# Kernel tuning notes

Hardware: AMD Instinct MI355X
Metric: run time of the kernel (lower is better)

Reference implementation:

```python
import jax, jax.numpy as jnp
import numpy as np

HEADS = 12
NUM_IMS = 1
SCALE = 1.0


def _layernorm(x, g, b, eps=1e-5):
    m = jnp.mean(x, axis=-1, keepdims=True)
    v = jnp.var(x, axis=-1, keepdims=True)
    return (x - m) / jnp.sqrt(v + eps) * g + b


def _mha(q, k, v):
    # q: [B, Nq, C], k/v: [B, Nk, C]; multi-head softmax attention
    B, Nq, C = q.shape
    d = C // HEADS
    qh = q.reshape(B, Nq, HEADS, d)
    kh = k.reshape(B, k.shape[1], HEADS, d)
    vh = v.reshape(B, v.shape[1], HEADS, d)
    sim = jnp.einsum('bihd,bjhd->bhij', qh, kh) * (d ** -0.5)
    w = jax.nn.softmax(sim, axis=-1)
    out = jnp.einsum('bhij,bjhd->bihd', w, vh)
    return out.reshape(B, Nq, C)


def _forward(hidden_states, encoder_hidden_states, ln1_g, ln1_b, ln2_g, ln2_b,
             sa_wq, sa_wk, sa_wv, sa_wo, sa_wo_b, ff_ln_g, ff_ln_b, ff_w1, ff_w2,
             alpha_attn, alpha_dense, ca_wq, ca_wk, ca_wv, ca_wo, ca_wo_b):
    B, N, C = hidden_states.shape
    end_pos = encoder_hidden_states.shape[1] - 16 * NUM_IMS
    text = encoder_hidden_states[:, :end_pos]   # [B, Lt, C]
    face = encoder_hidden_states[:, end_pos:]   # [B, 16, C]

    x = hidden_states
    # gated self-attention over visual tokens + face tokens
    x_ln = _layernorm(x, ln1_g, ln1_b)
    face_ln = _layernorm(face, ln1_g, ln1_b)
    comb = jnp.concatenate([x_ln, face_ln], axis=1)  # [B, N+16, C]
    attn_out = _mha(comb @ sa_wq, comb @ sa_wk, comb @ sa_wv) @ sa_wo + sa_wo_b
    attn_out = attn_out[:, :N]
    x = x + SCALE * jnp.tanh(alpha_attn) * attn_out

    # gated GEGLU feed-forward (norm2 outside, FF has its own LayerNorm)
    h = _layernorm(x, ln2_g, ln2_b)
    h = _layernorm(h, ff_ln_g, ff_ln_b)
    h = h @ ff_w1                                 # [B, N, 2*inner]
    a, gate = jnp.split(h, 2, axis=-1)
    h = (a * jax.nn.gelu(gate, approximate=False)) @ ff_w2
    x = x + SCALE * jnp.tanh(alpha_dense) * h

    residual = x
    # cross attention against text tokens (diffusers Attention, residual_connection=True)
    out = _mha(x @ ca_wq, text @ ca_wk, text @ ca_wv) @ ca_wo + ca_wo_b
    return out + residual


def setup_inputs() -> dict:
    key = jax.random.key(0)
    ks = jax.random.split(key, 16)
    B, N, C, L, INNER = 2, 1024, 768, 77 + 16 * NUM_IMS, 3072
    W = 0.02
    return {
        'hidden_states': jax.random.normal(ks[0], (B, N, C), jnp.float32),
        'encoder_hidden_states': jax.random.normal(ks[1], (B, L, C), jnp.float32),
        'ln1_g': jnp.ones((C,), jnp.float32),
        'ln1_b': jnp.zeros((C,), jnp.float32),
        'ln2_g': jnp.ones((C,), jnp.float32),
        'ln2_b': jnp.zeros((C,), jnp.float32),
        'sa_wq': jax.random.normal(ks[2], (C, C), jnp.float32) * W,
        'sa_wk': jax.random.normal(ks[3], (C, C), jnp.float32) * W,
        'sa_wv': jax.random.normal(ks[4], (C, C), jnp.float32) * W,
        'sa_wo': jax.random.normal(ks[5], (C, C), jnp.float32) * W,
        'sa_wo_b': jnp.zeros((C,), jnp.float32),
        'ff_ln_g': jnp.ones((C,), jnp.float32),
        'ff_ln_b': jnp.zeros((C,), jnp.float32),
        'ff_w1': jax.random.normal(ks[6], (C, 2 * INNER), jnp.float32) * W,
        'ff_w2': jax.random.normal(ks[7], (INNER, C), jnp.float32) * W,
        'alpha_attn': jnp.float32(0.5),
        'alpha_dense': jnp.float32(0.5),
        'ca_wq': jax.random.normal(ks[8], (C, C), jnp.float32) * W,
        'ca_wk': jax.random.normal(ks[9], (C, C), jnp.float32) * W,
        'ca_wv': jax.random.normal(ks[10], (C, C), jnp.float32) * W,
        'ca_wo': jax.random.normal(ks[11], (C, C), jnp.float32) * W,
        'ca_wo_b': jnp.zeros((C,), jnp.float32),
    }


def reference(hidden_states, encoder_hidden_states, ln1_g, ln1_b, ln2_g, ln2_b,
              sa_wq, sa_wk, sa_wv, sa_wo, sa_wo_b, ff_ln_g, ff_ln_b, ff_w1, ff_w2,
              alpha_attn, alpha_dense, ca_wq, ca_wk, ca_wv, ca_wo, ca_wo_b):
    return _forward(hidden_states, encoder_hidden_states, ln1_g, ln1_b, ln2_g, ln2_b,
                    sa_wq, sa_wk, sa_wv, sa_wo, sa_wo_b, ff_ln_g, ff_ln_b, ff_w1, ff_w2,
                    alpha_attn, alpha_dense, ca_wq, ca_wk, ca_wv, ca_wo, ca_wo_b)
```

## Files before the change

### kernel.cpp

```cpp
#include <hip/hip_runtime.h>
#include <hip/hip_bf16.h>
#include <math.h>


#define C_DIM 768
#define B_DIM 2
#define N_DIM 1024
#define NC_DIM 1040
#define L_DIM 93
#define TEXT_LEN 77
#define INNER 3072
#define MNX 1572864

typedef unsigned short ushort_t;
typedef __bf16 bf16x8 __attribute__((ext_vector_type(8)));
typedef float f32x4 __attribute__((ext_vector_type(4)));

__device__ __forceinline__ ushort_t f2b(float f) {
  __hip_bfloat16 h = __float2bfloat16(f);
  return *(ushort_t*)&h;
}
__device__ __forceinline__ float b2f(ushort_t u) {
  __hip_bfloat16 h = *(__hip_bfloat16*)&u;
  return __bfloat162float(h);
}

__device__ __forceinline__ void g2lds16(const void* g, void* l) {
  __builtin_amdgcn_global_load_lds(
      (const __attribute__((address_space(1))) unsigned int*)g,
      (__attribute__((address_space(3))) unsigned int*)l, 16, 0, 0);
}

#define WX1    0u
#define WX2    6291456u
#define WQKV   12582912u
#define WBB1   22167552u
#define WG     47333376u
#define WS1    59916288u
#define WTEXT  63062016u
#define WATT2  63298560u
#define WWQKV  66444288u
#define WWO    69983232u
#define WW1    71162880u
#define WW2    80600064u
#define WCAWQ  85318656u
#define WCAKV  86498304u
#define WCAWO  88857600u
#define WVT1   90037248u
#define WVT2   93379584u
#define WOPART WBB1
#define WLBUF  WG
#define WATTN  (WG + 524288u)
#define WPART  WBB1

__device__ __forceinline__ float block_sum(float v, float* sh) {
#pragma unroll
  for (int o = 32; o > 0; o >>= 1) v += __shfl_down(v, o);
  int lane = threadIdx.x & 63, w = threadIdx.x >> 6;
  if (lane == 0) sh[w] = v;
  __syncthreads();
  float r = sh[0] + sh[1] + sh[2] + sh[3];
  __syncthreads();
  return r;
}

struct WtDesc {
  const float* src[10];
  ushort_t*    dst[10];
  int K[10];
  int N[10];
  int tilesX[10];
  int ileave[10];
  int start[11];
};

__global__ __launch_bounds__(256)
void prep_kernel(WtDesc d,
                 const float* __restrict__ x, const float* __restrict__ enc,
                 const float* __restrict__ g, const float* __restrict__ b,
                 ushort_t* __restrict__ comb, ushort_t* __restrict__ text) {
  __shared__ float tile[64][65];
  int bid = blockIdx.x;
  int nwt = d.start[10];
  if (bid >= nwt) {
    int r = bid - nwt;
    if (r >= B_DIM * NC_DIM) {
      int i = r - B_DIM * NC_DIM;
      int bb = i / TEXT_LEN, j = i % TEXT_LEN;
      const float* src = enc + ((size_t)bb * L_DIM + j) * C_DIM;
      ushort_t* dst = text + (size_t)i * C_DIM;
#pragma unroll
      for (int l = 0; l < 3; ++l) {
        int c = threadIdx.x + l * 256;
        dst[c] = f2b(src[c]);
      }
      return;
    }
    float* sh = &tile[0][0];
    int bb = r / NC_DIM, i = r % NC_DIM;
    const float* src = (i < N_DIM)
        ? (x   + ((size_t)bb * N_DIM + i) * C_DIM)
        : (enc + ((size_t)bb * L_DIM + TEXT_LEN + (i - N_DIM)) * C_DIM);
    float v[3];
#pragma unroll
    for (int j = 0; j < 3; ++j) v[j] = src[threadIdx.x + j * 256];
    float mean = block_sum(v[0] + v[1] + v[2], sh) * (1.f / C_DIM);
    float sq = 0.f;
#pragma unroll
    for (int j = 0; j < 3; ++j) { float dd = v[j] - mean; sq += dd * dd; }
    float rstd = rsqrtf(block_sum(sq, sh) * (1.f / C_DIM) + 1e-5f);
    ushort_t* dst = comb + (size_t)r * C_DIM;
#pragma unroll
    for (int j = 0; j < 3; ++j) {
      int c = threadIdx.x + j * 256;
      dst[c] = f2b((v[j] - mean) * rstd * g[c] + b[c]);
    }
    return;
  }
  int j = 0;
  while (j < 9 && bid >= d.start[j + 1]) ++j;
  int ti = bid - d.start[j];
  int K = d.K[j], N = d.N[j];
  int n0 = (ti % d.tilesX[j]) * 64, k0 = (ti / d.tilesX[j]) * 64;
  const float* in = d.src[j];
  ushort_t* out = d.dst[j];
  int il = d.ileave[j];
  int t = threadIdx.x;
#pragma unroll
  for (int p = 0; p < 16; ++p) {
    int idx = t + p * 256;
    int r = idx >> 6, c = idx & 63;
    tile[r][c] = in[(size_t)(k0 + r) * N + n0 + c];
  }
  __syncthreads();
#pragma unroll
  for (int p = 0; p < 16; ++p) {
    int idx = t + p * 256;
    int r = idx >> 6, c = idx & 63;
    int nrow = n0 + r;
    int dstrow = il ? ((nrow < INNER) ? (nrow * 2) : ((nrow - INNER) * 2 + 1)) : nrow;
    out[(size_t)dstrow * K + k0 + c] = f2b(tile[c][r]);
  }
}

__global__ __launch_bounds__(256)
void gemm_bf16(const ushort_t* __restrict__ A, const ushort_t* __restrict__ Bt,
               ushort_t* __restrict__ Ob, ushort_t* __restrict__ Og,
               int M, int N, int K) {
  __shared__ ushort_t sA[2][128 * 32];
  __shared__ ushort_t sB[2][128 * 32];
  int t = threadIdx.x;
  int w = t >> 6, ln = t & 63;
  int m0 = blockIdx.y * 128, n0 = blockIdx.x * 128;
  int wm = (w >> 1) * 64, wn = (w & 1) * 64;
  int lr = ln & 15, lq = ln >> 4;
  int seg_r = ln >> 2, seg_c = (ln & 3) * 8;

  f32x4 acc[4][4];
#pragma unroll
  for (int mi = 0; mi < 4; ++mi)
#pragma unroll
    for (int ni = 0; ni < 4; ++ni) acc[mi][ni] = (f32x4){0.f, 0.f, 0.f, 0.f};

#define STAGE(k0_, buf_)                                                     \
  do {                                                                       \
    _Pragma("unroll") for (int l = 0; l < 2; ++l) {                          \
      int s = w * 2 + l;                                                     \
      int arow = m0 + s * 16 + seg_r;                                        \
      arow = arow < M ? arow : M - 1;                                        \
      g2lds16(A + (size_t)arow * K + (k0_) + seg_c, &sA[buf_][s * 512]);     \
      int nrow = n0 + s * 16 + seg_r;                                        \
      g2lds16(Bt + (size_t)nrow * K + (k0_) + seg_c, &sB[buf_][s * 512]);    \
    }                                                                        \
  } while (0)

  STAGE(0, 0);
  __syncthreads();
  int cur = 0;
  for (int k0 = 0; k0 < K; k0 += 32) {
    if (k0 + 32 < K) STAGE(k0 + 32, cur ^ 1);
    bf16x8 af[4], bfr[4];
#pragma unroll
    for (int mi = 0; mi < 4; ++mi)
      af[mi] = *(const bf16x8*)&sA[cur][(wm + mi * 16 + lr) * 32 + lq * 8];
#pragma unroll
    for (int ni = 0; ni < 4; ++ni)
      bfr[ni] = *(const bf16x8*)&sB[cur][(wn + ni * 16 + lr) * 32 + lq * 8];
#pragma unroll
    for (int mi = 0; mi < 4; ++mi)
#pragma unroll
      for (int ni = 0; ni < 4; ++ni)
        acc[mi][ni] = __builtin_amdgcn_mfma_f32_16x16x32_bf16(
            af[mi], bfr[ni], acc[mi][ni], 0, 0, 0);
    __syncthreads();
    cur ^= 1;
  }
#undef STAGE

  if (Og) {
#pragma unroll
    for (int mi = 0; mi < 4; ++mi)
#pragma unroll
      for (int ni = 0; ni < 4; ++ni) {
        int col = n0 + wn + ni * 16 + lr;
#pragma unroll
        for (int r = 0; r < 4; ++r) {
          float val = acc[mi][ni][r];
          float other = __shfl_xor(val, 1);
          if (!(lr & 1)) {
            float a = val, gate = other;
            float ge = 0.5f * gate * (1.f + erff(gate * 0.70710678118654752f));
            int row = m0 + wm + mi * 16 + lq * 4 + r;
            Og[(size_t)row * INNER + (col >> 1)] = f2b(a * ge);
          }
        }
      }
  } else {
#pragma unroll
    for (int mi = 0; mi < 4; ++mi)
#pragma unroll
      for (int ni = 0; ni < 4; ++ni) {
        int col = n0 + wn + ni * 16 + lr;
#pragma unroll
        for (int r = 0; r < 4; ++r) {
          int row = m0 + wm + mi * 16 + lq * 4 + r;
          if (row < M) Ob[(size_t)row * N + col] = f2b(acc[mi][ni][r]);
        }
      }
  }
}

__global__ __launch_bounds__(256)
void gemm64(const ushort_t* __restrict__ A, const ushort_t* __restrict__ Bt,
            float* __restrict__ Out, ushort_t* __restrict__ Ob,
            float* __restrict__ Part,
            int M, int N, int K, int Ksplit,
            const float* __restrict__ bias, const float* __restrict__ res,
            const float* __restrict__ alphaPtr,
            const ushort_t* __restrict__ A2, const ushort_t* __restrict__ Bt2,
            ushort_t* __restrict__ Ob2, int M2, int N2, int ybreak) {
  __shared__ ushort_t sA[2][4096];
  __shared__ ushort_t sB[2][4096];
  int by = blockIdx.y;
  if (A2 && by >= ybreak) {
    if ((int)blockIdx.x * 64 >= N2) return;
    A = A2; Bt = Bt2; Ob = Ob2; M = M2; N = N2;
    Out = nullptr; Part = nullptr; bias = nullptr; res = nullptr; alphaPtr = nullptr;
    by -= ybreak;
  }
  int t = threadIdx.x;
  int w = t >> 6, ln = t & 63;
  int m0 = by * 64, n0 = blockIdx.x * 64;
  int wm = (w >> 1) * 32, wn = (w & 1) * 32;
  int lr = ln & 15, lq = ln >> 4;
  int srow = (w & 1) * 32 + (ln >> 2);
  int skoff = (w >> 1) * 32 + (ln & 3) * 8;
  int kbeg = blockIdx.z * Ksplit;
  int kend = kbeg + Ksplit; if (kend > K) kend = K;

  f32x4 acc[2][2];
#pragma unroll
  for (int mi = 0; mi < 2; ++mi)
#pragma unroll
    for (int ni = 0; ni < 2; ++ni) acc[mi][ni] = (f32x4){0.f, 0.f, 0.f, 0.f};

#define STG64(k0_, buf_)                                                      \
  do {                                                                        \
    _Pragma("unroll") for (int i = 0; i < 2; ++i) {                           \
      int ar = m0 + srow + i * 16; ar = ar < M ? ar : M - 1;                  \
      g2lds16(A + (size_t)ar * K + (k0_) + skoff,                             \
              (char*)sA + (buf_) * 8192 + w * 2048 + i * 1024);               \
      int nr = n0 + srow + i * 16;                                            \
      g2lds16(Bt + (size_t)nr * K + (k0_) + skoff,                            \
              (char*)sB + (buf_) * 8192 + w * 2048 + i * 1024);               \
    }                                                                         \
  } while (0)

  STG64(kbeg, 0);
  __syncthreads();
  int cur = 0;
  for (int k0 = kbeg; k0 < kend; k0 += 64) {
    if (k0 + 64 < kend) STG64(k0 + 64, cur ^ 1);
#pragma unroll
    for (int s = 0; s < 2; ++s) {
      bf16x8 a0 = *(const bf16x8*)&sA[cur][s * 2048 + (wm + lr) * 32 + lq * 8];
      bf16x8 a1 = *(const bf16x8*)&sA[cur][s * 2048 + (wm + 16 + lr) * 32 + lq * 8];
      bf16x8 b0 = *(const bf16x8*)&sB[cur][s * 2048 + (wn + lr) * 32 + lq * 8];
      bf16x8 b1 = *(const bf16x8*)&sB[cur][s * 2048 + (wn + 16 + lr) * 32 + lq * 8];
      acc[0][0] = __builtin_amdgcn_mfma_f32_16x16x32_bf16(a0, b0, acc[0][0], 0, 0, 0);
      acc[0][1] = __builtin_amdgcn_mfma_f32_16x16x32_bf16(a0, b1, acc[0][1], 0, 0, 0);
      acc[1][0] = __builtin_amdgcn_mfma_f32_16x16x32_bf16(a1, b0, acc[1][0], 0, 0, 0);
      acc[1][1] = __builtin_amdgcn_mfma_f32_16x16x32_bf16(a1, b1, acc[1][1], 0, 0, 0);
    }
    __syncthreads();
    cur ^= 1;
  }
#undef STG64

  if (Part) {
    float* P = Part + (size_t)blockIdx.z * M * N;
#pragma unroll
    for (int mi = 0; mi < 2; ++mi)
#pragma unroll
      for (int ni = 0; ni < 2; ++ni) {
        int col = n0 + wn + ni * 16 + lr;
#pragma unroll
        for (int r = 0; r < 4; ++r) {
          int row = m0 + wm + mi * 16 + lq * 4 + r;
          if (row < M) P[(size_t)row * N + col] = acc[mi][ni][r];
        }
      }
  } else {
    float f = alphaPtr ? tanhf(alphaPtr[0]) : 1.0f;
#pragma unroll
    for (int mi = 0; mi < 2; ++mi)
#pragma unroll
      for (int ni = 0; ni < 2; ++ni) {
        int col = n0 + wn + ni * 16 + lr;
        float bv = bias ? bias[col] : 0.f;
#pragma unroll
        for (int r = 0; r < 4; ++r) {
          int row = m0 + wm + mi * 16 + lq * 4 + r;
          if (row < M) {
            float val = acc[mi][ni][r] + bv;
            if (res) val = res[(size_t)row * N + col] + f * val;
            if (Out) Out[(size_t)row * N + col] = val;
            if (Ob)  Ob[(size_t)row * N + col] = f2b(val);
          }
        }
      }
  }
}

__global__ __launch_bounds__(256)
void splitk_epi(const float* __restrict__ Part, int nz, float* __restrict__ Out,
                ushort_t* __restrict__ Ob, int MN, int N,
                const float* __restrict__ bias, const float* __restrict__ res,
                const float* __restrict__ alphaPtr) {
  int idx = (blockIdx.x * 256 + threadIdx.x) * 4;
  if (idx >= MN) return;
  float f = alphaPtr ? tanhf(alphaPtr[0]) : 1.0f;
  float v[4] = {0.f, 0.f, 0.f, 0.f};
  for (int z = 0; z < nz; ++z) {
    float4 a = *(const float4*)&Part[(size_t)z * MN + idx];
    v[0] += a.x; v[1] += a.y; v[2] += a.z; v[3] += a.w;
  }
  if (bias) {
    int col = idx % N;
    float4 bb = *(const float4*)&bias[col];
    v[0] += bb.x; v[1] += bb.y; v[2] += bb.z; v[3] += bb.w;
  }
  if (res) {
    float4 rr = *(const float4*)&res[idx];
    v[0] = rr.x + f * v[0]; v[1] = rr.y + f * v[1];
    v[2] = rr.z + f * v[2]; v[3] = rr.w + f * v[3];
  }
  if (Out) *(float4*)&Out[idx] = make_float4(v[0], v[1], v[2], v[3]);
  if (Ob) {
    ushort4 o;
    o.x = f2b(v[0]); o.y = f2b(v[1]); o.z = f2b(v[2]); o.w = f2b(v[3]);
    *(ushort4*)&Ob[idx] = o;
  }
}

__global__ __launch_bounds__(256)
void woepi_ln_kernel(const float* __restrict__ Part, int nz,
                     const float* __restrict__ bias, const float* __restrict__ xres,
                     const float* __restrict__ alphaPtr, float* __restrict__ x1,
                     const float* __restrict__ g1, const float* __restrict__ b1,
                     const float* __restrict__ g2, const float* __restrict__ b2,
                     ushort_t* __restrict__ hh) {
  __shared__ float sh[4];
  int row = blockIdx.x;
  float f = tanhf(alphaPtr[0]);
  float v[3];
#pragma unroll
  for (int j = 0; j < 3; ++j) {
    int c = threadIdx.x + j * 256;
    float s = 0.f;
    for (int z = 0; z < nz; ++z) s += Part[(size_t)z * MNX + (size_t)row * C_DIM + c];
    s += bias[c];
    float xv = xres[(size_t)row * C_DIM + c] + f * s;
    x1[(size_t)row * C_DIM + c] = xv;
    v[j] = xv;
  }
  float mean = block_sum(v[0] + v[1] + v[2], sh) * (1.f / C_DIM);
  float sq = 0.f;
#pragma unroll
  for (int j = 0; j < 3; ++j) { float d = v[j] - mean; sq += d * d; }
  float rstd = rsqrtf(block_sum(sq, sh) * (1.f / C_DIM) + 1e-5f);
  float y[3];
#pragma unroll
  for (int j = 0; j < 3; ++j) {
    int c = threadIdx.x + j * 256;
    y[j] = (v[j] - mean) * rstd * g1[c] + b1[c];
  }
  float mean2 = block_sum(y[0] + y[1] + y[2], sh) * (1.f / C_DIM);
  sq = 0.f;
#pragma unroll
  for (int j = 0; j < 3; ++j) { float d = y[j] - mean2; sq += d * d; }
  float rstd2 = rsqrtf(block_sum(sq, sh) * (1.f / C_DIM) + 1e-5f);
#pragma unroll
  for (int j = 0; j < 3; ++j) {
    int c = threadIdx.x + j * 256;
    hh[(size_t)row * C_DIM + c] = f2b((y[j] - mean2) * rstd2 * g2[c] + b2[c]);
  }
}

__global__ __launch_bounds__(256)
void vtrans_kernel(const ushort_t* __restrict__ V, ushort_t* __restrict__ Vt,
                   int rows_per_b, int stride, int Nk, int Nkp,
                   const ushort_t* __restrict__ V2, ushort_t* __restrict__ Vt2,
                   int rows2, int stride2, int Nk2, int Nkp2, int xbreak) {
  __shared__ ushort_t tile[64][68];
  int bx = blockIdx.x;
  if (bx >= xbreak) {
    bx -= xbreak;
    V = V2; Vt = Vt2; rows_per_b = rows2; stride = stride2; Nk = Nk2; Nkp = Nkp2;
  }
  int k0 = bx * 64;
  int h = blockIdx.y, b = blockIdx.z;
  int t = threadIdx.x;
#pragma unroll
  for (int p = 0; p < 4; ++p) {
    int r = p * 16 + (t >> 4), c = (t & 15) * 4;
    int key = k0 + r;
    ushort4 u = make_ushort4(0, 0, 0, 0);
    if (key < Nk)
      u = *(const ushort4*)&V[((size_t)(b * rows_per_b + key)) * stride + h * 64 + c];
    *(ushort4*)&tile[r][c] = u;
  }
  __syncthreads();
  size_t base = ((size_t)(b * 12 + h)) * 64 * Nkp;
#pragma unroll
  for (int p = 0; p < 4; ++p) {
    int dv = p * 16 + (t >> 4), kc = (t & 15) * 4;
    ushort4 u;
    u.x = tile[kc + 0][dv]; u.y = tile[kc + 1][dv];
    u.z = tile[kc + 2][dv]; u.w = tile[kc + 3][dv];
    *(ushort4*)&Vt[base + (size_t)dv * Nkp + k0 + kc] = u;
  }
}

__global__ __launch_bounds__(256)
void attn_mfma(const ushort_t* __restrict__ Q, const ushort_t* __restrict__ K,
               const ushort_t* __restrict__ Vt, ushort_t* __restrict__ O,
               float* __restrict__ Opart, float* __restrict__ lbuf,
               int q_rows_per_b, int kv_rows_per_b, int Nk, int Nkp,
               int qstride, int kstride, int nchunk) {
  __shared__ ushort_t sQ[4096];
  __shared__ ushort_t sK[2][4096];
  __shared__ ushort_t sV[2][4096];
  __shared__ ushort_t sP[4][1024];
  const float scale = 0.18033688011112042f;
  const float M0 = 16.0f;
  int t = threadIdx.x;
  int w = t >> 6, ln = t & 63;
  int col = ln & 15, quad = ln >> 4;
  int z = blockIdx.z;
  int b = z / nchunk, kc = z % nchunk;
  int h = blockIdx.y, q0 = blockIdx.x * 64;
  size_t vt_base = ((size_t)(b * 12 + h)) * 64 * Nkp;
  int ntiles = Nkp >> 6;
  int t0 = (kc * ntiles) / nchunk;
  int t1 = ((kc + 1) * ntiles) / nchunk;

#define STAGE_KV(kt_, bb_)                                                    \
  do {                                                                        \
    _Pragma("unroll") for (int s = 0; s < 2; ++s) {                           \
      int key = (kt_) * 64 + w * 16 + (ln >> 2);                              \
      g2lds16(K + (size_t)(b * kv_rows_per_b + key) * kstride                 \
                + h * 64 + s * 32 + (ln & 3) * 8,                             \
              (char*)sK[bb_] + s * 4096 + w * 1024);                          \
      int dv = w * 16 + (ln >> 2);                                            \
      g2lds16(Vt + vt_base + (size_t)dv * Nkp                                 \
                + (kt_) * 64 + s * 32 + (ln & 3) * 8,                         \
              (char*)sV[bb_] + s * 4096 + w * 1024);                          \
    }                                                                         \
  } while (0)

#pragma unroll
  for (int s = 0; s < 2; ++s) {
    int r = q0 + w * 16 + (ln >> 2);
    g2lds16(Q + (size_t)(b * q_rows_per_b + r) * qstride + h * 64 + s * 32 + (ln & 3) * 8,
            (char*)sQ + s * 4096 + w * 1024);
  }
  STAGE_KV(t0, 0);
  __syncthreads();
  bf16x8 qa[2];
#pragma unroll
  for (int s = 0; s < 2; ++s)
    qa[s] = *(const bf16x8*)&sQ[s * 2048 + (w * 16 + col) * 32 + quad * 8];

  f32x4 oacc[4];
#pragma unroll
  for (int i = 0; i < 4; ++i) oacc[i] = (f32x4){0.f, 0.f, 0.f, 0.f};
  float l_i[4] = {0.f, 0.f, 0.f, 0.f};

  ushort_t* sPw = sP[w];
  int bb = 0;

  for (int kt = t0; kt < t1; ++kt) {
    if (kt + 1 < t1) STAGE_KV(kt + 1, bb ^ 1);

    f32x4 cs[4];
#pragma unroll
    for (int nblk = 0; nblk < 4; ++nblk) {
      cs[nblk] = (f32x4){0.f, 0.f, 0.f, 0.f};
#pragma unroll
      for (int s = 0; s < 2; ++s) {
        bf16x8 kb = *(const bf16x8*)&sK[bb][s * 2048 + (nblk * 16 + col) * 32 + quad * 8];
        cs[nblk] = __builtin_amdgcn_mfma_f32_16x16x32_bf16(qa[s], kb, cs[nblk], 0, 0, 0);
      }
    }
    if (kt * 64 + 64 > Nk) {
#pragma unroll
      for (int nblk = 0; nblk < 4; ++nblk) {
        bool valid = (kt * 64 + nblk * 16 + col) < Nk;
#pragma unroll
        for (int r = 0; r < 4; ++r)
          cs[nblk][r] = valid ? cs[nblk][r] : -1e30f;
      }
    }
#pragma unroll
    for (int r = 0; r < 4; ++r) {
      int row = quad * 4 + r;
#pragma unroll
      for (int nblk = 0; nblk < 4; ++nblk) {
        float p = exp2f(fmaf(cs[nblk][r], scale, -M0));
        l_i[r] += p;
        int kin = (nblk & 1) * 16 + col;
        sPw[(nblk >> 1) * 512 + row * 32 + (kin ^ (quad << 3))] = f2b(p);
      }
    }
#pragma unroll
    for (int s = 0; s < 2; ++s) {
      bf16x8 pa = *(const bf16x8*)&sPw[s * 512 + col * 32 + ((quad ^ ((col >> 2) & 3)) << 3)];
#pragma unroll
      for (int nblk = 0; nblk < 4; ++nblk) {
        bf16x8 vb = *(const bf16x8*)&sV[bb][s * 2048 + (nblk * 16 + col) * 32 + quad * 8];
        oacc[nblk] = __builtin_amdgcn_mfma_f32_16x16x32_bf16(pa, vb, oacc[nblk], 0, 0, 0);
      }
    }
    if (kt + 1 < t1) __syncthreads();
    bb ^= 1;
  }
#undef STAGE_KV

#pragma unroll
  for (int r = 0; r < 4; ++r) {
    float ps = l_i[r];
#pragma unroll
    for (int o = 1; o < 16; o <<= 1) ps += __shfl_xor(ps, o);
    int qglob = b * N_DIM + q0 + w * 16 + quad * 4 + r;
    if (Opart) {
      if (col == 0) lbuf[(size_t)kc * (B_DIM * N_DIM * 12) + (size_t)qglob * 12 + h] = ps;
      float* op = Opart + (size_t)kc * MNX + (size_t)qglob * C_DIM + h * 64;
#pragma unroll
      for (int nblk = 0; nblk < 4; ++nblk)
        op[nblk * 16 + col] = oacc[nblk][r];
    } else {
      float inv = 1.f / ps;
#pragma unroll
      for (int nblk = 0; nblk < 4; ++nblk)
        O[(size_t)qglob * C_DIM + h * 64 + nblk * 16 + col] = f2b(oacc[nblk][r] * inv);
    }
  }
}

__global__ __launch_bounds__(256)
void attn_merge(const float* __restrict__ Opart, const float* __restrict__ lbuf,
                ushort_t* __restrict__ Ob, int nchunk) {
  int idx = (blockIdx.x * 256 + threadIdx.x) * 4;
  if (idx >= MNX) return;
  int row = idx / C_DIM, c = idx % C_DIM;
  int h = c >> 6;
  float l = 0.f;
  float v[4] = {0.f, 0.f, 0.f, 0.f};
  for (int kc = 0; kc < nchunk; ++kc) {
    l += lbuf[(size_t)kc * (B_DIM * N_DIM * 12) + (size_t)row * 12 + h];
    float4 p = *(const float4*)&Opart[(size_t)kc * MNX + idx];
    v[0] += p.x; v[1] += p.y; v[2] += p.z; v[3] += p.w;
  }
  float inv = 1.f / l;
  ushort4 o;
  o.x = f2b(v[0] * inv); o.y = f2b(v[1] * inv);
  o.z = f2b(v[2] * inv); o.w = f2b(v[3] * inv);
  *(ushort4*)&Ob[idx] = o;
}

extern "C" void kernel_launch(void* const* d_in, const int* in_sizes, int n_in,
                              void* d_out, int out_size, void* d_ws, size_t ws_size,
                              hipStream_t stream) {
  const float* x        = (const float*)d_in[0];
  const float* enc      = (const float*)d_in[1];
  const float* ln1_g    = (const float*)d_in[2];
  const float* ln1_b    = (const float*)d_in[3];
  const float* ln2_g    = (const float*)d_in[4];
  const float* ln2_b    = (const float*)d_in[5];
  const float* sa_wq    = (const float*)d_in[6];
  const float* sa_wk    = (const float*)d_in[7];
  const float* sa_wv    = (const float*)d_in[8];
  const float* sa_wo    = (const float*)d_in[9];
  const float* sa_wo_b  = (const float*)d_in[10];
  const float* ff_ln_g  = (const float*)d_in[11];
  const float* ff_ln_b  = (const float*)d_in[12];
  const float* ff_w1    = (const float*)d_in[13];
  const float* ff_w2    = (const float*)d_in[14];
  const float* a_attn   = (const float*)d_in[15];
  const float* a_dense  = (const float*)d_in[16];
  const float* ca_wq    = (const float*)d_in[17];
  const float* ca_wk    = (const float*)d_in[18];
  const float* ca_wv    = (const float*)d_in[19];
  const float* ca_wo    = (const float*)d_in[20];
  const float* ca_wo_b  = (const float*)d_in[21];

  char* ws = (char*)d_ws;
  float*    x1     = (float*)(ws + WX1);
  float*    x2     = (float*)(ws + WX2);
  ushort_t* qkv_b  = (ushort_t*)(ws + WQKV);
  ushort_t* q2b    = (ushort_t*)(ws + WQKV);
  ushort_t* kv2b   = (ushort_t*)(ws + WQKV + 3145728u);
  ushort_t* comb_b = (ushort_t*)(ws + WBB1);
  float*    opart  = (float*)(ws + WOPART);
  float*    lbuf   = (float*)(ws + WLBUF);
  ushort_t* attn_b = (ushort_t*)(ws + WATTN);
  ushort_t* g_b    = (ushort_t*)(ws + WG);
  ushort_t* hh     = (ushort_t*)(ws + WS1);
  ushort_t* x2b    = (ushort_t*)(ws + WS1);
  ushort_t* text_b = (ushort_t*)(ws + WTEXT);
  ushort_t* attn2b = (ushort_t*)(ws + WATT2);
  ushort_t* wqkv_t = (ushort_t*)(ws + WWQKV);
  ushort_t* wo_t   = (ushort_t*)(ws + WWO);
  ushort_t* w1_t   = (ushort_t*)(ws + WW1);
  ushort_t* w2_t   = (ushort_t*)(ws + WW2);
  ushort_t* cawq_t = (ushort_t*)(ws + WCAWQ);
  ushort_t* cakv_t = (ushort_t*)(ws + WCAKV);
  ushort_t* cawo_t = (ushort_t*)(ws + WCAWO);
  ushort_t* vt1    = (ushort_t*)(ws + WVT1);
  ushort_t* vt2    = (ushort_t*)(ws + WVT2);
  float* part = (float*)(ws + WPART);
  float* out = (float*)d_out;

  const int Mc = B_DIM * NC_DIM;
  const int Mx = B_DIM * N_DIM;
  const int Mt = B_DIM * TEXT_LEN;

  WtDesc wd;
  const float* srcs[10] = {sa_wq, sa_wk, sa_wv, sa_wo, ca_wq, ca_wk, ca_wv, ca_wo, ff_w1, ff_w2};
  ushort_t* dsts[10] = {wqkv_t, wqkv_t + 589824, wqkv_t + 2 * 589824, wo_t,
                        cawq_t, cakv_t, cakv_t + 589824, cawo_t, w1_t, w2_t};
  int Ks[10] = {768, 768, 768, 768, 768, 768, 768, 768, 768, 3072};
  int Ns[10] = {768, 768, 768, 768, 768, 768, 768, 768, 6144, 768};
  int total = 0;
  for (int j = 0; j < 10; ++j) {
    wd.src[j] = srcs[j]; wd.dst[j] = dsts[j];
    wd.K[j] = Ks[j]; wd.N[j] = Ns[j];
    wd.tilesX[j] = Ns[j] / 64;
    wd.ileave[j] = (j == 8) ? 1 : 0;
    wd.start[j] = total;
    total += (Ns[j] / 64) * (Ks[j] / 64);
  }
  wd.start[10] = total;

  prep_kernel<<<total + Mc + Mt, 256, 0, stream>>>(
      wd, x, enc, ln1_g, ln1_b, comb_b, text_b);
  gemm64<<<dim3(36, 36, 1), 256, 0, stream>>>(
      comb_b, wqkv_t, nullptr, qkv_b, nullptr, Mc, 2304, 768, 768,
      nullptr, nullptr, nullptr,
      text_b, cakv_t, kv2b, Mt, 1536, 33);
  vtrans_kernel<<<dim3(19, 12, B_DIM), 256, 0, stream>>>(
      qkv_b + 1536, vt1, NC_DIM, 2304, NC_DIM, 1088,
      kv2b + 768, vt2, TEXT_LEN, 1536, TEXT_LEN, 128, 17);
  attn_mfma<<<dim3(N_DIM / 64, 12, B_DIM * 2), 256, 0, stream>>>(
      qkv_b + 0, qkv_b + 768, vt1, nullptr, opart, lbuf,
      NC_DIM, NC_DIM, NC_DIM, 1088, 2304, 2304, 2);
  attn_merge<<<MNX / 1024, 256, 0, stream>>>(opart, lbuf, attn_b, 2);
  gemm64<<<dim3(12, 32, 2), 256, 0, stream>>>(
      attn_b, wo_t, nullptr, nullptr, part, Mx, 768, 768, 384,
      nullptr, nullptr, nullptr,
      nullptr, nullptr, nullptr, 0, 0, 0);
  woepi_ln_kernel<<<Mx, 256, 0, stream>>>(
      part, 2, sa_wo_b, x, a_attn, x1, ln2_g, ln2_b, ff_ln_g, ff_ln_b, hh);
  gemm_bf16<<<dim3(48, 16), 256, 0, stream>>>(
      hh, w1_t, nullptr, g_b, Mx, 6144, 768);
  gemm64<<<dim3(12, 32, 2), 256, 0, stream>>>(
      g_b, w2_t, nullptr, nullptr, part, Mx, 768, 3072, 1536,
      nullptr, nullptr, nullptr,
      nullptr, nullptr, nullptr, 0, 0, 0);
  splitk_epi<<<MNX / 1024, 256, 0, stream>>>(
      part, 2, x2, x2b, MNX, 768, nullptr, x1, a_dense);
  gemm64<<<dim3(12, 32, 1), 256, 0, stream>>>(
      x2b, cawq_t, nullptr, q2b, nullptr, Mx, 768, 768, 768,
      nullptr, nullptr, nullptr,
      nullptr, nullptr, nullptr, 0, 0, 0);
  attn_mfma<<<dim3(N_DIM / 64, 12, B_DIM), 256, 0, stream>>>(
      q2b, kv2b + 0, vt2, attn2b, nullptr, nullptr,
      N_DIM, TEXT_LEN, TEXT_LEN, 128, 768, 1536, 1);
  gemm64<<<dim3(12, 32, 1), 256, 0, stream>>>(
      attn2b, cawo_t, out, nullptr, nullptr, Mx, 768, 768, 768,
      ca_wo_b, x2, nullptr,
      nullptr, nullptr, nullptr, 0, 0, 0);
}
```

Baseline: 304.5 us.

## Drop split-KV self-attention merge and run FF2 on split-K 128x128 GEMM

Self-attention now runs one block per (query tile, head, batch) over all keys, and writes normalized bf16 output directly. This removes the two-chunk partial output buffers and the separate attn_merge kernel, but halves the number of attention blocks. The second feed-forward GEMM moves from the 64-tile gemm64 with 2-way split-K to the 128x128 gemm_bf16 with a new 4-way split-K partial-store path. The split-K epilogue now reduces 4 partials, which adds partial-buffer traffic in exchange for larger tiles.

New measurement: 305.7 us. No clear change (+0.4%).

```diff
diff --git a/kernel.cpp b/kernel.cpp
--- a/kernel.cpp
+++ b/kernel.cpp
@@ -48,8 +48,6 @@
 #define WCAWO  88857600u
 #define WVT1   90037248u
 #define WVT2   93379584u
-#define WOPART WBB1
-#define WLBUF  WG
 #define WATTN  (WG + 524288u)
 #define WPART  WBB1
 
@@ -146,7 +144,8 @@
 __global__ __launch_bounds__(256)
 void gemm_bf16(const ushort_t* __restrict__ A, const ushort_t* __restrict__ Bt,
                ushort_t* __restrict__ Ob, ushort_t* __restrict__ Og,
-               int M, int N, int K) {
+               float* __restrict__ Part,
+               int M, int N, int K, int Ksplit) {
   __shared__ ushort_t sA[2][128 * 32];
   __shared__ ushort_t sB[2][128 * 32];
   int t = threadIdx.x;
@@ -155,6 +154,8 @@
   int wm = (w >> 1) * 64, wn = (w & 1) * 64;
   int lr = ln & 15, lq = ln >> 4;
   int seg_r = ln >> 2, seg_c = (ln & 3) * 8;
+  int kbeg = blockIdx.z * Ksplit;
+  int kend = kbeg + Ksplit; if (kend > K) kend = K;
 
   f32x4 acc[4][4];
 #pragma unroll
@@ -174,11 +175,11 @@
     }                                                                        \
   } while (0)
 
-  STAGE(0, 0);
+  STAGE(kbeg, 0);
   __syncthreads();
   int cur = 0;
-  for (int k0 = 0; k0 < K; k0 += 32) {
-    if (k0 + 32 < K) STAGE(k0 + 32, cur ^ 1);
+  for (int k0 = kbeg; k0 < kend; k0 += 32) {
+    if (k0 + 32 < kend) STAGE(k0 + 32, cur ^ 1);
     bf16x8 af[4], bfr[4];
 #pragma unroll
     for (int mi = 0; mi < 4; ++mi)
@@ -197,7 +198,20 @@
   }
 #undef STAGE
 
-  if (Og) {
+  if (Part) {
+    float* P = Part + (size_t)blockIdx.z * M * N;
+#pragma unroll
+    for (int mi = 0; mi < 4; ++mi)
+#pragma unroll
+      for (int ni = 0; ni < 4; ++ni) {
+        int col = n0 + wn + ni * 16 + lr;
+#pragma unroll
+        for (int r = 0; r < 4; ++r) {
+          int row = m0 + wm + mi * 16 + lq * 4 + r;
+          if (row < M) P[(size_t)row * N + col] = acc[mi][ni][r];
+        }
+      }
+  } else if (Og) {
 #pragma unroll
     for (int mi = 0; mi < 4; ++mi)
 #pragma unroll
@@ -445,9 +459,8 @@
 __global__ __launch_bounds__(256)
 void attn_mfma(const ushort_t* __restrict__ Q, const ushort_t* __restrict__ K,
                const ushort_t* __restrict__ Vt, ushort_t* __restrict__ O,
-               float* __restrict__ Opart, float* __restrict__ lbuf,
                int q_rows_per_b, int kv_rows_per_b, int Nk, int Nkp,
-               int qstride, int kstride, int nchunk) {
+               int qstride, int kstride) {
   __shared__ ushort_t sQ[4096];
   __shared__ ushort_t sK[2][4096];
   __shared__ ushort_t sV[2][4096];
@@ -457,13 +470,10 @@
   int t = threadIdx.x;
   int w = t >> 6, ln = t & 63;
   int col = ln & 15, quad = ln >> 4;
-  int z = blockIdx.z;
-  int b = z / nchunk, kc = z % nchunk;
+  int b = blockIdx.z;
   int h = blockIdx.y, q0 = blockIdx.x * 64;
   size_t vt_base = ((size_t)(b * 12 + h)) * 64 * Nkp;
   int ntiles = Nkp >> 6;
-  int t0 = (kc * ntiles) / nchunk;
-  int t1 = ((kc + 1) * ntiles) / nchunk;
 
 #define STAGE_KV(kt_, bb_)                                                    \
   do {                                                                        \
@@ -485,7 +495,7 @@
     g2lds16(Q + (size_t)(b * q_rows_per_b + r) * qstride + h * 64 + s * 32 + (ln & 3) * 8,
             (char*)sQ + s * 4096 + w * 1024);
   }
-  STAGE_KV(t0, 0);
+  STAGE_KV(0, 0);
   __syncthreads();
   bf16x8 qa[2];
 #pragma unroll
@@ -500,8 +510,8 @@
   ushort_t* sPw = sP[w];
   int bb = 0;
 
-  for (int kt = t0; kt < t1; ++kt) {
-    if (kt + 1 < t1) STAGE_KV(kt + 1, bb ^ 1);
+  for (int kt = 0; kt < ntiles; ++kt) {
+    if (kt + 1 < ntiles) STAGE_KV(kt + 1, bb ^ 1);
 
     f32x4 cs[4];
 #pragma unroll
@@ -542,7 +552,7 @@
         oacc[nblk] = __builtin_amdgcn_mfma_f32_16x16x32_bf16(pa, vb, oacc[nblk], 0, 0, 0);
       }
     }
-    if (kt + 1 < t1) __syncthreads();
+    if (kt + 1 < ntiles) __syncthreads();
     bb ^= 1;
   }
 #undef STAGE_KV
@@ -553,40 +563,11 @@
 #pragma unroll
     for (int o = 1; o < 16; o <<= 1) ps += __shfl_xor(ps, o);
     int qglob = b * N_DIM + q0 + w * 16 + quad * 4 + r;
-    if (Opart) {
-      if (col == 0) lbuf[(size_t)kc * (B_DIM * N_DIM * 12) + (size_t)qglob * 12 + h] = ps;
-      float* op = Opart + (size_t)kc * MNX + (size_t)qglob * C_DIM + h * 64;
-#pragma unroll
-      for (int nblk = 0; nblk < 4; ++nblk)
-        op[nblk * 16 + col] = oacc[nblk][r];
-    } else {
-      float inv = 1.f / ps;
-#pragma unroll
-      for (int nblk = 0; nblk < 4; ++nblk)
-        O[(size_t)qglob * C_DIM + h * 64 + nblk * 16 + col] = f2b(oacc[nblk][r] * inv);
-    }
-  }
-}
-
-__global__ __launch_bounds__(256)
-void attn_merge(const float* __restrict__ Opart, const float* __restrict__ lbuf,
-                ushort_t* __restrict__ Ob, int nchunk) {
-  int idx = (blockIdx.x * 256 + threadIdx.x) * 4;
-  if (idx >= MNX) return;
-  int row = idx / C_DIM, c = idx % C_DIM;
-  int h = c >> 6;
-  float l = 0.f;
-  float v[4] = {0.f, 0.f, 0.f, 0.f};
-  for (int kc = 0; kc < nchunk; ++kc) {
-    l += lbuf[(size_t)kc * (B_DIM * N_DIM * 12) + (size_t)row * 12 + h];
-    float4 p = *(const float4*)&Opart[(size_t)kc * MNX + idx];
-    v[0] += p.x; v[1] += p.y; v[2] += p.z; v[3] += p.w;
-  }
-  float inv = 1.f / l;
-  ushort4 o;
-  o.x = f2b(v[0] * inv); o.y = f2b(v[1] * inv);
-  o.z = f2b(v[2] * inv); o.w = f2b(v[3] * inv);
-  *(ushort4*)&Ob[idx] = o;
+    float inv = 1.f / ps;
+#pragma unroll
+    for (int nblk = 0; nblk < 4; ++nblk)
+      O[(size_t)qglob * C_DIM + h * 64 + nblk * 16 + col] = f2b(oacc[nblk][r] * inv);
+  }
 }
 
 extern "C" void kernel_launch(void* const* d_in, const int* in_sizes, int n_in,
@@ -622,8 +603,6 @@
   ushort_t* q2b    = (ushort_t*)(ws + WQKV);
   ushort_t* kv2b   = (ushort_t*)(ws + WQKV + 3145728u);
   ushort_t* comb_b = (ushort_t*)(ws + WBB1);
-  float*    opart  = (float*)(ws + WOPART);
-  float*    lbuf   = (float*)(ws + WLBUF);
   ushort_t* attn_b = (ushort_t*)(ws + WATTN);
   ushort_t* g_b    = (ushort_t*)(ws + WG);
   ushort_t* hh     = (ushort_t*)(ws + WS1);
@@ -672,31 +651,28 @@
   vtrans_kernel<<<dim3(19, 12, B_DIM), 256, 0, stream>>>(
       qkv_b + 1536, vt1, NC_DIM, 2304, NC_DIM, 1088,
       kv2b + 768, vt2, TEXT_LEN, 1536, TEXT_LEN, 128, 17);
-  attn_mfma<<<dim3(N_DIM / 64, 12, B_DIM * 2), 256, 0, stream>>>(
-      qkv_b + 0, qkv_b + 768, vt1, nullptr, opart, lbuf,
-      NC_DIM, NC_DIM, NC_DIM, 1088, 2304, 2304, 2);
-  attn_merge<<<MNX / 1024, 256, 0, stream>>>(opart, lbuf, attn_b, 2);
+  attn_mfma<<<dim3(N_DIM / 64, 12, B_DIM), 256, 0, stream>>>(
+      qkv_b + 0, qkv_b + 768, vt1, attn_b,
+      NC_DIM, NC_DIM, NC_DIM, 1088, 2304, 2304);
   gemm64<<<dim3(12, 32, 2), 256, 0, stream>>>(
       attn_b, wo_t, nullptr, nullptr, part, Mx, 768, 768, 384,
       nullptr, nullptr, nullptr,
       nullptr, nullptr, nullptr, 0, 0, 0);
   woepi_ln_kernel<<<Mx, 256, 0, stream>>>(
       part, 2, sa_wo_b, x, a_attn, x1, ln2_g, ln2_b, ff_ln_g, ff_ln_b, hh);
-  gemm_bf16<<<dim3(48, 16), 256, 0, stream>>>(
-      hh, w1_t, nullptr, g_b, Mx, 6144, 768);
-  gemm64<<<dim3(12, 32, 2), 256, 0, stream>>>(
-      g_b, w2_t, nullptr, nullptr, part, Mx, 768, 3072, 1536,
-      nullptr, nullptr, nullptr,
-      nullptr, nullptr, nullptr, 0, 0, 0);
+  gemm_bf16<<<dim3(48, 16, 1), 256, 0, stream>>>(
+      hh, w1_t, nullptr, g_b, nullptr, Mx, 6144, 768, 768);
+  gemm_bf16<<<dim3(6, 16, 4), 256, 0, stream>>>(
+      g_b, w2_t, nullptr, nullptr, part, Mx, 768, 3072, 768);
   splitk_epi<<<MNX / 1024, 256, 0, stream>>>(
-      part, 2, x2, x2b, MNX, 768, nullptr, x1, a_dense);
+      part, 4, x2, x2b, MNX, 768, nullptr, x1, a_dense);
   gemm64<<<dim3(12, 32, 1), 256, 0, stream>>>(
       x2b, cawq_t, nullptr, q2b, nullptr, Mx, 768, 768, 768,
       nullptr, nullptr, nullptr,
       nullptr, nullptr, nullptr, 0, 0, 0);
   attn_mfma<<<dim3(N_DIM / 64, 12, B_DIM), 256, 0, stream>>>(
-      q2b, kv2b + 0, vt2, attn2b, nullptr, nullptr,
-      N_DIM, TEXT_LEN, TEXT_LEN, 128, 768, 1536, 1);
+      q2b, kv2b + 0, vt2, attn2b,
+      N_DIM, TEXT_LEN, TEXT_LEN, 128, 768, 1536);
   gemm64<<<dim3(12, 32, 1), 256, 0, stream>>>(
       attn2b, cawo_t, out, nullptr, nullptr, Mx, 768, 768, 768,
       ca_wo_b, x2, nullptr,
```
